# Optimization experiments

Hardware: AMD Instinct MI355X
Metric: run time of the kernel (lower is better)

Reference implementation:

```python
import jax, jax.numpy as jnp
import numpy as np


def setup_inputs() -> dict:
    key = jax.random.key(0)
    k1, k2 = jax.random.split(key)
    B, C, D = 8192, 8192, 256
    x = jax.random.normal(k1, (B, D), dtype=jnp.float32)
    y = jax.random.normal(k2, (C, D), dtype=jnp.float32)
    gamma = jnp.ones((), dtype=jnp.float32)
    return {"x": x, "y": y, "gamma": gamma}


def reference(x, y, gamma):
    # RBF kernel: exp(-gamma * ||x_i - y_j||^2), shape (B, C).
    # avoiding the O(B*C*D) broadcast-diff intermediate of the naive form.
    x2 = jnp.sum(x * x, axis=-1)          # (B,)
    y2 = jnp.sum(y * y, axis=-1)          # (C,)
    xy = jnp.einsum('bd,cd->bc', x, y)    # (B, C) GEMM
    sq_dist = x2[:, None] + y2[None, :] - 2.0 * xy
    sq_dist = jnp.maximum(sq_dist, 0.0)   # guard tiny negatives from cancellation
    return jnp.exp(-gamma * sq_dist)
```

## Files before the change

### kernel.cpp

```cpp
#include <hip/hip_runtime.h>
#include <hip/hip_bf16.h>

typedef __bf16 bf16_t;
typedef __attribute__((ext_vector_type(8))) __bf16 bf16x8;
typedef __attribute__((ext_vector_type(4))) __bf16 bf16x4;
typedef __attribute__((ext_vector_type(4))) float floatx4;

#define NB 8192
#define NC 8192
#define ND 256
#define NKT 8
#define BM 128
#define BN 128

__global__ __launch_bounds__(256) void prep_kernel(
    const float* __restrict__ x, const float* __restrict__ y,
    bf16_t* __restrict__ xs, bf16_t* __restrict__ ys,
    float* __restrict__ x2, float* __restrict__ y2)
{
    int t    = threadIdx.x;
    int wave = t >> 6;
    int lane = t & 63;
    int row  = blockIdx.x * 4 + wave;

    const float* src;
    bf16_t* dst;
    float* nrm;
    int r;
    if (row < NB) { src = x; dst = xs; nrm = x2; r = row; }
    else          { src = y; dst = ys; nrm = y2; r = row - NB; }

    float4 v = ((const float4*)(src + (size_t)r * ND))[lane];
    float ss = v.x * v.x + v.y * v.y + v.z * v.z + v.w * v.w;

    bf16x4 o;
    o.x = (__bf16)v.x; o.y = (__bf16)v.y; o.z = (__bf16)v.z; o.w = (__bf16)v.w;

    const int g  = r >> 4;
    const int rr = r & 15;
    const int kt = lane >> 3;
    const int q  = (lane >> 1) & 3;
    const int h  = (lane & 1) * 8;
    char* p = (char*)dst + (((size_t)(g * NKT + kt)) << 10) + q * 256 + rr * 16 + h;
    *(bf16x4*)p = o;

    #pragma unroll
    for (int off = 32; off >= 1; off >>= 1)
        ss += __shfl_xor(ss, off, 64);
    if (lane == 0) nrm[r] = ss;
}

__global__ __launch_bounds__(256) void rbf_gemm_kernel(
    const bf16_t* __restrict__ xs, const bf16_t* __restrict__ ys,
    const float* __restrict__ x2, const float* __restrict__ y2,
    const float* __restrict__ gamma_p, float* __restrict__ out)
{
    const int t    = threadIdx.x;
    const int lane = t & 63;
    const int wave = t >> 6;
    const int wm   = wave >> 1;
    const int wn   = wave & 1;
    const int quad = lane >> 4;
    const int l15  = lane & 15;

    const int bm = blockIdx.x * BM;
    const int bn = blockIdx.y * BN;

    const float gamma = *gamma_p;

    floatx4 acc[4][4];
    #pragma unroll
    for (int i = 0; i < 4; ++i)
        #pragma unroll
        for (int j = 0; j < 4; ++j)
            acc[i][j] = (floatx4){0.f, 0.f, 0.f, 0.f};

    const char* aBase = (const char*)xs
        + (((size_t)((bm >> 4) + wm * 4) * NKT) << 10) + (size_t)lane * 16;
    const char* bBase = (const char*)ys
        + (((size_t)((bn >> 4) + wn * 4) * NKT) << 10) + (size_t)lane * 16;

    bf16x8 af[2][4], bfv[2][4];
    auto ldset = [&](int kt, int buf) {
        #pragma unroll
        for (int i = 0; i < 4; ++i) {
            af[buf][i]  = *(const bf16x8*)(aBase + i * (NKT * 1024) + kt * 1024);
            bfv[buf][i] = *(const bf16x8*)(bBase + i * (NKT * 1024) + kt * 1024);
        }
    };

    ldset(0, 0);
    #pragma unroll
    for (int kt = 0; kt < NKT; ++kt) {
        const int cb = kt & 1;
        if (kt + 1 < NKT) ldset(kt + 1, cb ^ 1);
        #pragma unroll
        for (int i = 0; i < 4; ++i)
            #pragma unroll
            for (int j = 0; j < 4; ++j)
                acc[i][j] = __builtin_amdgcn_mfma_f32_16x16x32_bf16(
                    af[cb][i], bfv[cb][j], acc[i][j], 0, 0, 0);
    }

    #pragma unroll
    for (int i = 0; i < 4; ++i) {
        const int grow0 = bm + wm * 64 + i * 16 + quad * 4;
        const float4 xn = *(const float4*)(x2 + grow0);
        #pragma unroll
        for (int j = 0; j < 4; ++j) {
            const int gcol = bn + wn * 64 + j * 16 + l15;
            const float yn = y2[gcol];
            float* op = out + (size_t)grow0 * NC + gcol;
            const float xr[4] = {xn.x, xn.y, xn.z, xn.w};
            #pragma unroll
            for (int r = 0; r < 4; ++r) {
                float sq = xr[r] + yn - 2.0f * acc[i][j][r];
                sq = fmaxf(sq, 0.0f);
                __builtin_nontemporal_store(__expf(-gamma * sq),
                                            op + (size_t)r * NC);
            }
        }
    }
}

extern "C" void kernel_launch(void* const* d_in, const int* in_sizes, int n_in,
                              void* d_out, int out_size, void* d_ws, size_t ws_size,
                              hipStream_t stream) {
    const float* x = (const float*)d_in[0];
    const float* y = (const float*)d_in[1];
    const float* gamma = (const float*)d_in[2];
    float* out = (float*)d_out;

    bf16_t* xs = (bf16_t*)d_ws;
    bf16_t* ys = xs + (size_t)NB * ND;
    float*  x2 = (float*)(ys + (size_t)NC * ND);
    float*  y2 = x2 + NB;

    prep_kernel<<<dim3((NB + NC) / 4), dim3(256), 0, stream>>>(x, y, xs, ys, x2, y2);
    rbf_gemm_kernel<<<dim3(NB / BM, NC / BN), dim3(256), 0, stream>>>(
        xs, ys, x2, y2, gamma, out);
}
```

Measured before the change: 327.9 us.

## Stage epilogue through LDS for vectorized stores and remap blocks per XCD

The epilogue now writes exp results into a per-wave shared-memory tile and reads them back as float4 rows, so each global store is a 16-byte nontemporal write covering contiguous columns instead of scattered scalar stores. The grid is flattened to 1D and block IDs are remapped so that each of the 8 XCDs gets a contiguous 16x32 region of output tiles, aiming for better L2 reuse of xs/ys. This adds LDS traffic and about 17KB of shared memory per block, which may reduce occupancy.

```diff
diff --git a/kernel.cpp b/kernel.cpp
--- a/kernel.cpp
+++ b/kernel.cpp
@@ -55,6 +55,8 @@
     const float* __restrict__ x2, const float* __restrict__ y2,
     const float* __restrict__ gamma_p, float* __restrict__ out)
 {
+    __shared__ float et[4][16][68];
+
     const int t    = threadIdx.x;
     const int lane = t & 63;
     const int wave = t >> 6;
@@ -63,8 +65,15 @@
     const int quad = lane >> 4;
     const int l15  = lane & 15;
 
-    const int bm = blockIdx.x * BM;
-    const int bn = blockIdx.y * BN;
+    const int fid = blockIdx.x;
+    const int xcd = fid & 7;
+    const int lid = fid >> 3;
+    const int sr  = xcd >> 1;
+    const int sc  = xcd & 1;
+    const int cr  = lid >> 5;
+    const int cc  = lid & 31;
+    const int bm  = (sr * 16 + cr) * BM;
+    const int bn  = (sc * 32 + cc) * BN;
 
     const float gamma = *gamma_p;
 
@@ -102,23 +111,29 @@
                     af[cb][i], bfv[cb][j], acc[i][j], 0, 0, 0);
     }
 
+    float (*ew)[68] = et[wave];
+    const int colbase = bn + wn * 64;
     #pragma unroll
     for (int i = 0; i < 4; ++i) {
-        const int grow0 = bm + wm * 64 + i * 16 + quad * 4;
-        const float4 xn = *(const float4*)(x2 + grow0);
+        const int grow0 = bm + wm * 64 + i * 16;
+        const float4 xn = *(const float4*)(x2 + grow0 + quad * 4);
+        const float xr[4] = {xn.x, xn.y, xn.z, xn.w};
         #pragma unroll
         for (int j = 0; j < 4; ++j) {
-            const int gcol = bn + wn * 64 + j * 16 + l15;
-            const float yn = y2[gcol];
-            float* op = out + (size_t)grow0 * NC + gcol;
-            const float xr[4] = {xn.x, xn.y, xn.z, xn.w};
+            const float yn = y2[colbase + j * 16 + l15];
             #pragma unroll
             for (int r = 0; r < 4; ++r) {
                 float sq = xr[r] + yn - 2.0f * acc[i][j][r];
                 sq = fmaxf(sq, 0.0f);
-                __builtin_nontemporal_store(__expf(-gamma * sq),
-                                            op + (size_t)r * NC);
+                ew[quad * 4 + r][j * 16 + l15] = __expf(-gamma * sq);
             }
+        }
+        #pragma unroll
+        for (int c = 0; c < 4; ++c) {
+            const int rr = c * 4 + quad;
+            floatx4 v = *(const floatx4*)&ew[rr][l15 * 4];
+            __builtin_nontemporal_store(
+                v, (floatx4*)(out + (size_t)(grow0 + rr) * NC + colbase + l15 * 4));
         }
     }
 }
@@ -137,6 +152,6 @@
     float*  y2 = x2 + NB;
 
     prep_kernel<<<dim3((NB + NC) / 4), dim3(256), 0, stream>>>(x, y, xs, ys, x2, y2);
-    rbf_gemm_kernel<<<dim3(NB / BM, NC / BN), dim3(256), 0, stream>>>(
+    rbf_gemm_kernel<<<dim3((NB / BM) * (NC / BN)), dim3(256), 0, stream>>>(
         xs, ys, x2, y2, gamma, out);
 }
```

Measured after the change: 315.5 us. 3.8% less time.
